# Kernel optimization log

Hardware: AMD Instinct MI355X
Metric: run time of the kernel (lower is better)

Reference implementation:

```python
import jax, jax.numpy as jnp
import numpy as np
from jax import lax

# static dims (match init_kwargs)
B, F, C, H, W = 10, 64, 3, 180, 180   # batch=10 (hard-coded by reshape), arr_size frames
CH, OUT, NCLS = 64, 256, 5            # channel, out_size, len(ansmap)+1
K1, K2, POOL = 9, 5, 2                # second*diff, third, pool
EPS = 1e-5


def setup_inputs() -> dict:
    key = jax.random.key(0)
    ks = jax.random.split(key, 12)
    s = lambda k, shape: jax.random.normal(k, shape, dtype=jnp.float32) * 0.05
    return {
        "x": jax.random.normal(ks[0], (B, F, C, H, W), dtype=jnp.float32),
        "W1": s(ks[1], (CH, C, K1, K1)),
        "b1": s(ks[2], (CH,)),
        "W2": s(ks[3], (3, CH, K2, K2)),
        "b2": s(ks[4], (3,)),
        "gamma": jnp.ones((F,), jnp.float32),
        "beta": jnp.zeros((F,), jnp.float32),
        "Wih": s(ks[5], (3, OUT, 1)),
        "Whh": s(ks[6], (3, OUT, OUT)),
        "bih": s(ks[7], (3, OUT)),
        "bhh": s(ks[8], (3, OUT)),
        "Wl": s(ks[9], (NCLS, OUT)),
        "bl": s(ks[10], (NCLS,)),
    }


def _maxpool2(y):
    return lax.reduce_window(y, -jnp.inf, lax.max, (1, 1, POOL, POOL), (1, 1, POOL, POOL), 'VALID')


def reference(x, W1, b1, W2, b2, gamma, beta, Wih, Whh, bih, bhh, Wl, bl):
    # conv stack applied per frame; batch all B*F frames at once
    xc = x.reshape(B * F, C, H, W)
    y = lax.conv_general_dilated(xc, W1, (K1, K1), 'VALID') + b1[None, :, None, None]
    y = _maxpool2(jax.nn.relu(y))                      # [B*F, CH, 10, 10]
    y = lax.conv_general_dilated(y, W2, (K2, K2), 'VALID') + b2[None, :, None, None]
    y = _maxpool2(jax.nn.relu(y))                      # [B*F, 3, 1, 1]
    y = y.reshape(B, F, 3)

    # BatchNorm1d(arr_size) in train mode: normalize each of the F channels over (batch, length)
    mean = y.mean(axis=(0, 2), keepdims=True)
    var = y.var(axis=(0, 2), keepdims=True)
    y = (y - mean) / jnp.sqrt(var + EPS) * gamma[None, :, None] + beta[None, :, None]

    # per-sample reorder of the 3 channels by (max - min) range over time
    t = y.transpose(0, 2, 1)                           # [B, 3, F]
    rng = t.max(-1) - t.min(-1)                        # [B, 3]
    perm = jnp.argsort(rng, axis=1)                    # [B, 3]
    ts = jnp.take_along_axis(t, perm[:, :, None], axis=1)  # [B, 3, F]

    # rank r goes through RNN r; vmap the scan over the 3 RNNs
    seqs = ts.transpose(1, 2, 0)[..., None]            # [3, F, B, 1]

    def rnn_last(seq, wih, whh, bi, bh):               # seq: [F, B, 1]
        def step(h, xt):
            return jnp.tanh(xt @ wih.T + bi + h @ whh.T + bh), None
        h, _ = lax.scan(step, jnp.zeros((B, OUT), seq.dtype), seq)
        return h                                       # last hidden == output at t=-1

    lasts = jax.vmap(rnn_last)(seqs, Wih, Whh, bih, bhh)  # [3, B, OUT]
    avg = lasts.mean(axis=0)                           # AvgPool2d((3,1)) + Flatten -> [B, OUT]
    return avg @ Wl.T + bl                             # [B, NCLS]
```

## Files before the change

kernel.cpp:

```cpp
#include <hip/hip_runtime.h>

typedef __attribute__((ext_vector_type(8))) short bf16x8;
typedef __attribute__((ext_vector_type(4))) float f32x4;

#define MFMA16(a,b,c) __builtin_amdgcn_mfma_f32_16x16x32_bf16((a),(b),(c),0,0,0)

#define AS1 __attribute__((address_space(1)))
#define AS3 __attribute__((address_space(3)))
__device__ __forceinline__ void async16(void* lds, const void* g){
  __builtin_amdgcn_global_load_lds((const AS1 unsigned int*)g, (AS3 unsigned int*)lds, 16, 0, 0);
}

__device__ __forceinline__ unsigned short f2bf(float f){
  unsigned int u = __float_as_uint(f);
  unsigned int r = (u + 0x7fffu + ((u>>16)&1u)) >> 16;
  return (unsigned short)r;
}
__device__ __forceinline__ float bf2f(unsigned short h){
  return __uint_as_float(((unsigned int)h)<<16);
}
__device__ __forceinline__ float tanh_fast(float x){
  float e = __expf(2.f*x);
  return 1.f - 2.f/(e + 1.f);
}

#define WS_W1H   0u
#define WS_W1L   32768u
#define WS_WHHH  65536u
#define WS_WHHL  458752u
#define WS_Y1    851968u
#define WS_Y2    17235968u
#define WS_LAST  17255936u

__global__ __launch_bounds__(256) void k_prep(const float* __restrict__ W1,
                                              const float* __restrict__ Whh,
                                              unsigned short* __restrict__ w1h,
                                              unsigned short* __restrict__ w1l,
                                              unsigned short* __restrict__ whh_h,
                                              unsigned short* __restrict__ whh_l){
  int t = blockIdx.x*256 + threadIdx.x;
  if (t < 2048){
    int l = t & 63, kt = (t>>6)&7, mt = t>>9;
    int co = mt*16 + (l&15);
    int k0 = kt*32 + ((l>>4)<<3);
    bf16x8 hv, lv;
    #pragma unroll
    for (int j=0;j<8;j++){
      int k = k0 + j;
      float v = (k < 243) ? W1[co*243 + k] : 0.f;
      unsigned short h = f2bf(v);
      unsigned short lo = f2bf(v - bf2f(h));
      hv[j] = (short)h; lv[j] = (short)lo;
    }
    *(bf16x8*)(w1h + (size_t)t*8) = hv;
    *(bf16x8*)(w1l + (size_t)t*8) = lv;
  } else if (t < 2048 + 24576){
    int u = t - 2048;
    int l = u & 63, kt = (u>>6)&7, nt = (u>>9)&15, rnn = u>>13;
    int o = nt*16 + (l&15);
    int k0 = kt*32 + ((l>>4)<<3);
    const float* src = Whh + ((size_t)rnn*256 + o)*256;
    bf16x8 hv, lv;
    #pragma unroll
    for (int j=0;j<8;j++){
      float v = src[k0 + j];
      unsigned short h = f2bf(v);
      unsigned short lo = f2bf(v - bf2f(h));
      hv[j] = (short)h; lv[j] = (short)lo;
    }
    *(bf16x8*)(whh_h + (size_t)u*8) = hv;
    *(bf16x8*)(whh_l + (size_t)u*8) = lv;
  }
}

__global__ __launch_bounds__(256,2) void k_conv1(const float* __restrict__ x,
                                                 const float* __restrict__ b1,
                                                 const unsigned short* __restrict__ w1h,
                                                 const unsigned short* __restrict__ w1l,
                                                 float* __restrict__ y1){
  __shared__ __align__(16) char smem[79840];
  int fr = blockIdx.x / 10, g = blockIdx.x % 10;
  int t = threadIdx.x, w = t>>6, l = t&63;

  const float4* xb4 = (const float4*)x + (size_t)fr*24300 + (size_t)g*810;
  for (int i=t; i<2430; i+=256){
    int c = i/810;
    int rem = i - c*810;
    async16(smem + 40960 + i*16, (const void*)(xb4 + c*8100 + rem));
  }

  bf16x8 ah[8], al[8];
  #pragma unroll
  for (int kt=0; kt<8; kt++){
    size_t fi = (((size_t)(w*8 + kt))*64 + l)*8;
    ah[kt] = *(const bf16x8*)(w1h + fi);
    al[kt] = *(const bf16x8*)(w1l + fi);
  }
  float bias[4];
  #pragma unroll
  for (int reg=0;reg<4;reg++) bias[reg] = b1[w*16 + ((l>>4)<<2) + reg];

  for (int i=t; i<520; i+=256){
    int p = i/13, k = 243 + (i - p*13);
    int off = ((p<<9) + (k<<1)) ^ ((p&7)<<4);
    *(unsigned short*)(smem + off) = 0;
    *(unsigned short*)(smem + 20480 + off) = 0;
  }
  __syncthreads();

  for (int i=t; i<2430; i+=256){
    int c = i/810;
    int rem = i - c*810;
    int rl = rem/45;
    int quad = rem - rl*45;
    int oyl = (rl >= 9) ? 1 : 0;
    int ky = rl - 9*oyl;
    float4 v4 = *(const float4*)(smem + 40960 + i*16);
    int kbase = c*81 + ky*9;
    int col0 = quad<<2;
    int ox = (col0*57)>>9;
    int kx = col0 - 9*ox;
    int p = oyl*20 + ox;
    float vv[4] = {v4.x, v4.y, v4.z, v4.w};
    #pragma unroll
    for (int q=0;q<4;q++){
      int k = kbase + kx;
      int off = ((p<<9) + (k<<1)) ^ ((p&7)<<4);
      unsigned int u = __float_as_uint(vv[q]);
      *(unsigned short*)(smem + off) = (unsigned short)(u>>16);
      float lof = vv[q] - __uint_as_float(u & 0xffff0000u);
      *(unsigned short*)(smem + 20480 + off) = (unsigned short)(__float_as_uint(lof)>>16);
      kx++; if (kx==9){ kx=0; p++; }
    }
  }
  __syncthreads();

  const int pbase[3] = {0, 16, 24};
  int colb = (l>>4)<<4;
  f32x4 acc[3];
  #pragma unroll
  for (int nt=0;nt<3;nt++) acc[nt] = (f32x4){0.f,0.f,0.f,0.f};
  #pragma unroll
  for (int nt=0; nt<3; nt++){
    int p = pbase[nt] + (l&15);
    int sw = (p&7)<<4;
    #pragma unroll
    for (int kt=0; kt<8; kt++){
      int off = ((p<<9) + (kt<<6) + colb) ^ sw;
      bf16x8 bh  = *(const bf16x8*)(smem + off);
      bf16x8 blo = *(const bf16x8*)(smem + 20480 + off);
      acc[nt] = MFMA16(ah[kt], bh,  acc[nt]);
      acc[nt] = MFMA16(ah[kt], blo, acc[nt]);
      acc[nt] = MFMA16(al[kt], bh,  acc[nt]);
    }
  }
  __syncthreads();

  float* poolb = (float*)smem;
  #pragma unroll
  for (int nt=0;nt<3;nt++){
    int m = l&15;
    int p = pbase[nt] + m;
    #pragma unroll
    for (int reg=0;reg<4;reg++){
      int co = w*16 + ((l>>4)<<2) + reg;
      float v = fmaxf(acc[nt][reg] + bias[reg], 0.f);
      if (nt != 2 || m >= 8) poolb[co*41 + p] = v;
    }
  }
  __syncthreads();
  for (int idx=t; idx<640; idx+=256){
    int co = idx/10, xp = idx - co*10;
    const float* pb = poolb + co*41;
    float m = fmaxf(fmaxf(pb[2*xp], pb[2*xp+1]), fmaxf(pb[20+2*xp], pb[21+2*xp]));
    y1[(size_t)fr*6400 + co*100 + g*10 + xp] = m;
  }
}

__global__ __launch_bounds__(256) void k_conv2(const float* __restrict__ y1,
                                               const float* __restrict__ W2,
                                               const float* __restrict__ b2,
                                               float* __restrict__ y2){
  __shared__ __align__(16) float yl[6400];
  __shared__ __align__(16) float w2s[4800];
  int fr = blockIdx.x, t = threadIdx.x;
  const float4* src = (const float4*)(y1 + (size_t)fr*6400);
  for (int i=t;i<1600;i+=256) async16(((float4*)yl) + i, (const void*)(src + i));
  for (int i=t;i<1200;i+=256) async16(((float4*)w2s) + i, (const void*)(((const float4*)W2) + i));
  __syncthreads();
  if (t < 192){
    int o = t>>4, l16 = t&15;
    int ch = o>>2, pos = o&3;
    int oy = pos>>1, ox = pos&1;
    float s = 0.f;
    for (int i=0;i<100;i++){
      int k = l16 + (i<<4);
      int ci = k/25; int r = k - ci*25; int ky = r/5, kx = r - ky*5;
      s += yl[ci*100 + (5*oy+ky)*10 + 5*ox + kx] * w2s[ch*1600 + k];
    }
    #pragma unroll
    for (int d=1; d<16; d<<=1) s += __shfl_xor(s, d);
    float v = fmaxf(s + b2[ch], 0.f);
    v = fmaxf(v, __shfl_xor(v, 16));
    v = fmaxf(v, __shfl_xor(v, 32));
    if ((t&63)==0) y2[fr*3 + (t>>6)] = v;
  }
}

__global__ __launch_bounds__(512) void k_rnn(const unsigned short* __restrict__ whh_h,
                                             const unsigned short* __restrict__ whh_l,
                                             const float* __restrict__ y2,
                                             const float* __restrict__ gamma,
                                             const float* __restrict__ beta,
                                             const float* __restrict__ Wih,
                                             const float* __restrict__ bih,
                                             const float* __restrict__ bhh,
                                             float* __restrict__ lasts){
  __shared__ __align__(16) char hsm[36864];
  float* yl   = (float*)hsm;
  float* af   = (float*)(hsm + 7680);
  float* bfv  = (float*)(hsm + 7936);
  float* rngL = (float*)(hsm + 8192);
  int*   perm = (int*)(hsm + 8320);
  float* tsb  = (float*)(hsm + 8448);
  float* seqL = (float*)(hsm + 32768);
  int rnn = blockIdx.x;
  int t = threadIdx.x, w = t>>6, l = t&63;

  bf16x8 Bh[2][8], Bl[2][8];
  #pragma unroll
  for (int q=0;q<2;q++){
    int nt = 2*w + q;
    #pragma unroll
    for (int kt=0;kt<8;kt++){
      size_t fi = (((((size_t)rnn*16 + nt)*8) + kt)*64 + l)*8;
      Bh[q][kt] = *(const bf16x8*)(whh_h + fi);
      Bl[q][kt] = *(const bf16x8*)(whh_l + fi);
    }
  }
  int o0 = (2*w)*16 + (l&15), o1 = o0 + 16;
  float wih0 = Wih[rnn*256 + o0], wih1 = Wih[rnn*256 + o1];
  float bs0 = bih[rnn*256+o0] + bhh[rnn*256+o0];
  float bs1 = bih[rnn*256+o1] + bhh[rnn*256+o1];

  for (int i=t;i<1920;i+=512) yl[i] = y2[i];
  __syncthreads();
  if (t < 64){
    float mu = 0.f;
    for (int b=0;b<10;b++)
      for (int ch=0;ch<3;ch++) mu += yl[(b*64 + t)*3 + ch];
    mu *= (1.f/30.f);
    float v = 0.f;
    for (int b=0;b<10;b++)
      for (int ch=0;ch<3;ch++){ float d = yl[(b*64+t)*3+ch] - mu; v += d*d; }
    v *= (1.f/30.f);
    float rs = rsqrtf(v + 1e-5f);
    float a = gamma[t]*rs;
    af[t] = a; bfv[t] = beta[t] - mu*a;
  }
  __syncthreads();
  if (t < 30){
    int b = t/3, ch = t - b*3;
    float mx = -1e30f, mn = 1e30f;
    for (int f=0; f<64; f++){
      float v = yl[(b*64+f)*3+ch]*af[f] + bfv[f];
      tsb[(b*3+ch)*64 + f] = v;
      mx = fmaxf(mx, v); mn = fminf(mn, v);
    }
    rngL[b*3+ch] = mx - mn;
  }
  __syncthreads();
  if (t < 10){
    #pragma unroll
    for (int ch=0; ch<3; ch++){
      float rc = rngL[t*3+ch];
      int rank = 0;
      #pragma unroll
      for (int c2=0; c2<3; c2++){
        float r2 = rngL[t*3+c2];
        if (r2 < rc || (r2 == rc && c2 < ch)) rank++;
      }
      perm[t*3+rank] = ch;
    }
  }
  __syncthreads();
  for (int i=t;i<1024;i+=512){
    int step = i>>4, b = i&15;
    float v = 0.f;
    if (b < 10){ int p = perm[b*3 + rnn]; v = tsb[(b*3+p)*64 + step]; }
    seqL[i] = v;
  }
  __syncthreads();

  float4 z4 = {0.f,0.f,0.f,0.f};
  for (int i=t; i<1024; i+=512) ((float4*)hsm)[i] = z4;
  __syncthreads();
  int arow = l&15, colb = (l>>4)<<4, sw = (arow&7)<<4;
  int b_base = (l>>4)<<2;
  for (int step=0; step<64; step++){
    char* cur = hsm + ((step&1)<<14);
    char* nxt = hsm + (((step+1)&1)<<14);
    f32x4 p0=(f32x4){0,0,0,0}, q0=p0, r0=p0, p1=p0, q1=p0, r1=p0;
    #pragma unroll
    for (int kt=0; kt<8; kt++){
      int off = ((arow<<9) + (kt<<6) + colb) ^ sw;
      bf16x8 ahv = *(const bf16x8*)(cur + off);
      bf16x8 alv = *(const bf16x8*)(cur + 8192 + off);
      p0 = MFMA16(ahv, Bh[0][kt], p0);
      q0 = MFMA16(ahv, Bl[0][kt], q0);
      r0 = MFMA16(alv, Bh[0][kt], r0);
      p1 = MFMA16(ahv, Bh[1][kt], p1);
      q1 = MFMA16(ahv, Bl[1][kt], q1);
      r1 = MFMA16(alv, Bh[1][kt], r1);
    }
    float4 sx = *(const float4*)(seqL + (step<<4) + b_base);
    float sxa[4] = {sx.x, sx.y, sx.z, sx.w};
    #pragma unroll
    for (int reg=0; reg<4; reg++){
      int b = b_base + reg;
      float a0 = (p0[reg] + q0[reg]) + r0[reg];
      float a1 = (p1[reg] + q1[reg]) + r1[reg];
      float h0 = tanh_fast(a0 + sxa[reg]*wih0 + bs0);
      float h1 = tanh_fast(a1 + sxa[reg]*wih1 + bs1);
      int wsw = (b&7)<<4;
      int off0 = ((b<<9) + (o0<<1)) ^ wsw;
      int off1 = ((b<<9) + (o1<<1)) ^ wsw;
      unsigned int u0 = __float_as_uint(h0);
      unsigned int u1 = __float_as_uint(h1);
      *(unsigned short*)(nxt + off0) = (unsigned short)(u0>>16);
      float l0 = h0 - __uint_as_float(u0 & 0xffff0000u);
      *(unsigned short*)(nxt + 8192 + off0) = (unsigned short)(__float_as_uint(l0)>>16);
      *(unsigned short*)(nxt + off1) = (unsigned short)(u1>>16);
      float l1 = h1 - __uint_as_float(u1 & 0xffff0000u);
      *(unsigned short*)(nxt + 8192 + off1) = (unsigned short)(__float_as_uint(l1)>>16);
      if (step == 63){
        lasts[((size_t)rnn*16 + b)*256 + o0] = h0;
        lasts[((size_t)rnn*16 + b)*256 + o1] = h1;
      }
    }
    __syncthreads();
  }
}

__global__ __launch_bounds__(512) void k_head(const float* __restrict__ lasts,
                                              const float* __restrict__ Wl,
                                              const float* __restrict__ bl,
                                              float* __restrict__ out){
  int t = threadIdx.x;
  if (t < 400){
    int oidx = t>>3, l8 = t&7;
    int b = oidx/5, c = oidx - b*5;
    float s = 0.f;
    for (int i=0;i<32;i++){
      int o = (l8<<5) + i;
      float avg = (lasts[(size_t)(0*16+b)*256+o] + lasts[(size_t)(1*16+b)*256+o]
                 + lasts[(size_t)(2*16+b)*256+o]) * (1.f/3.f);
      s += avg * Wl[c*256 + o];
    }
    #pragma unroll
    for (int d=1; d<8; d<<=1) s += __shfl_xor(s, d);
    if (l8 == 0) out[oidx] = s + bl[c];
  }
}

extern "C" void kernel_launch(void* const* d_in, const int* in_sizes, int n_in,
                              void* d_out, int out_size, void* d_ws, size_t ws_size,
                              hipStream_t stream){
  const float* x    = (const float*)d_in[0];
  const float* W1   = (const float*)d_in[1];
  const float* b1   = (const float*)d_in[2];
  const float* W2   = (const float*)d_in[3];
  const float* b2   = (const float*)d_in[4];
  const float* gamma= (const float*)d_in[5];
  const float* beta = (const float*)d_in[6];
  const float* Wih  = (const float*)d_in[7];
  const float* Whh  = (const float*)d_in[8];
  const float* bih  = (const float*)d_in[9];
  const float* bhh  = (const float*)d_in[10];
  const float* Wl   = (const float*)d_in[11];
  const float* bl   = (const float*)d_in[12];
  char* ws = (char*)d_ws;
  unsigned short* w1h  = (unsigned short*)(ws + WS_W1H);
  unsigned short* w1l  = (unsigned short*)(ws + WS_W1L);
  unsigned short* whhh = (unsigned short*)(ws + WS_WHHH);
  unsigned short* whhl = (unsigned short*)(ws + WS_WHHL);
  float* y1   = (float*)(ws + WS_Y1);
  float* y2   = (float*)(ws + WS_Y2);
  float* last = (float*)(ws + WS_LAST);

  hipLaunchKernelGGL(k_prep,  dim3(104),  dim3(256), 0, stream, W1, Whh, w1h, w1l, whhh, whhl);
  hipLaunchKernelGGL(k_conv1, dim3(6400), dim3(256), 0, stream, x, b1, w1h, w1l, y1);
  hipLaunchKernelGGL(k_conv2, dim3(640),  dim3(256), 0, stream, y1, W2, b2, y2);
  hipLaunchKernelGGL(k_rnn,   dim3(3),    dim3(512), 0, stream, whhh, whhl, y2, gamma, beta, Wih, bih, bhh, last);
  hipLaunchKernelGGL(k_head,  dim3(1),    dim3(512), 0, stream, last, Wl, bl, (float*)d_out);
}
```

Baseline: 204.2 us.

## Shrink conv1 LDS footprint by processing output rows in two halves with register prefetch

The conv1 kernel now stages only one output row (20 positions) of im2col data at a time, cutting shared memory from about 80KB to 20KB and raising the launch-bounds occupancy hint from 2 to 8 blocks. Input is loaded straight into registers instead of being copied into an LDS staging buffer, and the second row's loads are issued before the first row's MFMAs to overlap latency. Max-pooling now uses lane shuffles and a register max across the two row passes, replacing the LDS pool buffer. The cost is more registers per thread, an extra barrier round, and two MFMA passes that each cover two overlapping position tiles.

```diff
diff --git a/kernel.cpp b/kernel.cpp
--- a/kernel.cpp
+++ b/kernel.cpp
@@ -73,107 +73,157 @@
   }
 }
 
-__global__ __launch_bounds__(256,2) void k_conv1(const float* __restrict__ x,
+__global__ __launch_bounds__(256,8) void k_conv1(const float* __restrict__ x,
                                                  const float* __restrict__ b1,
                                                  const unsigned short* __restrict__ w1h,
                                                  const unsigned short* __restrict__ w1l,
                                                  float* __restrict__ y1){
-  __shared__ __align__(16) char smem[79840];
-  int fr = blockIdx.x / 10, g = blockIdx.x % 10;
+  __shared__ __align__(16) char smem[20480];
+  int fr = blockIdx.x/10, g = blockIdx.x%10;
   int t = threadIdx.x, w = t>>6, l = t&63;
 
-  const float4* xb4 = (const float4*)x + (size_t)fr*24300 + (size_t)g*810;
-  for (int i=t; i<2430; i+=256){
-    int c = i/810;
-    int rem = i - c*810;
-    async16(smem + 40960 + i*16, (const void*)(xb4 + c*8100 + rem));
-  }
-
   bf16x8 ah[8], al[8];
   #pragma unroll
-  for (int kt=0; kt<8; kt++){
-    size_t fi = (((size_t)(w*8 + kt))*64 + l)*8;
-    ah[kt] = *(const bf16x8*)(w1h + fi);
-    al[kt] = *(const bf16x8*)(w1l + fi);
+  for (int kt=0;kt<8;kt++){
+    size_t fi = (((size_t)(w*8+kt))*64 + l)*8;
+    ah[kt] = *(const bf16x8*)(w1h+fi);
+    al[kt] = *(const bf16x8*)(w1l+fi);
   }
   float bias[4];
   #pragma unroll
   for (int reg=0;reg<4;reg++) bias[reg] = b1[w*16 + ((l>>4)<<2) + reg];
 
-  for (int i=t; i<520; i+=256){
-    int p = i/13, k = 243 + (i - p*13);
-    int off = ((p<<9) + (k<<1)) ^ ((p&7)<<4);
-    *(unsigned short*)(smem + off) = 0;
-    *(unsigned short*)(smem + 20480 + off) = 0;
-  }
-  __syncthreads();
-
-  for (int i=t; i<2430; i+=256){
-    int c = i/810;
-    int rem = i - c*810;
-    int rl = rem/45;
-    int quad = rem - rl*45;
-    int oyl = (rl >= 9) ? 1 : 0;
-    int ky = rl - 9*oyl;
-    float4 v4 = *(const float4*)(smem + 40960 + i*16);
-    int kbase = c*81 + ky*9;
+  const float4* xb = (const float4*)x + (size_t)fr*24300;
+  int rowbase = g*18;
+
+  float4 rv[5]; int pp[5], kk[5], kxv[5]; bool okv[5];
+  #pragma unroll
+  for (int ii=0; ii<5; ii++){
+    int i = t + (ii<<8);
+    okv[ii] = (i < 1215);
+    int c = i/405, rem = i - c*405;
+    int ky = rem/45, quad = rem - ky*45;
     int col0 = quad<<2;
     int ox = (col0*57)>>9;
-    int kx = col0 - 9*ox;
-    int p = oyl*20 + ox;
-    float vv[4] = {v4.x, v4.y, v4.z, v4.w};
-    #pragma unroll
-    for (int q=0;q<4;q++){
-      int k = kbase + kx;
-      int off = ((p<<9) + (k<<1)) ^ ((p&7)<<4);
-      unsigned int u = __float_as_uint(vv[q]);
-      *(unsigned short*)(smem + off) = (unsigned short)(u>>16);
-      float lof = vv[q] - __uint_as_float(u & 0xffff0000u);
-      *(unsigned short*)(smem + 20480 + off) = (unsigned short)(__float_as_uint(lof)>>16);
-      kx++; if (kx==9){ kx=0; p++; }
-    }
-  }
-  __syncthreads();
-
-  const int pbase[3] = {0, 16, 24};
-  int colb = (l>>4)<<4;
-  f32x4 acc[3];
-  #pragma unroll
-  for (int nt=0;nt<3;nt++) acc[nt] = (f32x4){0.f,0.f,0.f,0.f};
-  #pragma unroll
-  for (int nt=0; nt<3; nt++){
-    int p = pbase[nt] + (l&15);
-    int sw = (p&7)<<4;
-    #pragma unroll
-    for (int kt=0; kt<8; kt++){
-      int off = ((p<<9) + (kt<<6) + colb) ^ sw;
-      bf16x8 bh  = *(const bf16x8*)(smem + off);
-      bf16x8 blo = *(const bf16x8*)(smem + 20480 + off);
-      acc[nt] = MFMA16(ah[kt], bh,  acc[nt]);
-      acc[nt] = MFMA16(ah[kt], blo, acc[nt]);
-      acc[nt] = MFMA16(al[kt], bh,  acc[nt]);
-    }
-  }
-  __syncthreads();
-
-  float* poolb = (float*)smem;
-  #pragma unroll
-  for (int nt=0;nt<3;nt++){
-    int m = l&15;
-    int p = pbase[nt] + m;
-    #pragma unroll
-    for (int reg=0;reg<4;reg++){
-      int co = w*16 + ((l>>4)<<2) + reg;
-      float v = fmaxf(acc[nt][reg] + bias[reg], 0.f);
-      if (nt != 2 || m >= 8) poolb[co*41 + p] = v;
-    }
-  }
-  __syncthreads();
-  for (int idx=t; idx<640; idx+=256){
-    int co = idx/10, xp = idx - co*10;
-    const float* pb = poolb + co*41;
-    float m = fmaxf(fmaxf(pb[2*xp], pb[2*xp+1]), fmaxf(pb[20+2*xp], pb[21+2*xp]));
-    y1[(size_t)fr*6400 + co*100 + g*10 + xp] = m;
+    kxv[ii] = col0 - 9*ox;
+    pp[ii] = ox;
+    kk[ii] = c*81 + ky*9;
+    int gi = c*8100 + (rowbase + ky)*45 + quad;
+    rv[ii] = okv[ii] ? xb[gi] : (float4){0.f,0.f,0.f,0.f};
+  }
+  for (int i=t; i<260; i+=256){
+    int p = i/13, k = 243 + (i - p*13);
+    int off = ((p<<9)+(k<<1)) ^ ((p&7)<<4);
+    *(unsigned short*)(smem+off) = 0;
+    *(unsigned short*)(smem+10240+off) = 0;
+  }
+  #pragma unroll
+  for (int ii=0; ii<5; ii++){
+    if (okv[ii]){
+      int p = pp[ii], kx = kxv[ii];
+      float vv[4] = {rv[ii].x, rv[ii].y, rv[ii].z, rv[ii].w};
+      #pragma unroll
+      for (int q=0;q<4;q++){
+        int k = kk[ii] + kx;
+        int off = ((p<<9)+(k<<1)) ^ ((p&7)<<4);
+        unsigned int u = __float_as_uint(vv[q]);
+        *(unsigned short*)(smem+off) = (unsigned short)(u>>16);
+        float lof = vv[q] - __uint_as_float(u & 0xffff0000u);
+        *(unsigned short*)(smem+10240+off) = (unsigned short)(__float_as_uint(lof)>>16);
+        kx++; if (kx==9){ kx=0; p++; }
+      }
+    }
+  }
+  __syncthreads();
+
+  #pragma unroll
+  for (int ii=0; ii<5; ii++){
+    int i = t + (ii<<8);
+    int c = i/405, rem = i - c*405;
+    int ky = rem/45, quad = rem - ky*45;
+    int gi = c*8100 + (rowbase + 9 + ky)*45 + quad;
+    rv[ii] = okv[ii] ? xb[gi] : (float4){0.f,0.f,0.f,0.f};
+  }
+
+  int m = l&15, colb = (l>>4)<<4;
+  int p0 = m, p1 = 4+m;
+  int sw0 = (p0&7)<<4, sw1 = (p1&7)<<4;
+  f32x4 acc0 = (f32x4){0.f,0.f,0.f,0.f}, acc1 = acc0;
+  #pragma unroll
+  for (int kt=0;kt<8;kt++){
+    int off0 = ((p0<<9)+(kt<<6)+colb) ^ sw0;
+    int off1 = ((p1<<9)+(kt<<6)+colb) ^ sw1;
+    bf16x8 bh0 = *(const bf16x8*)(smem+off0);
+    bf16x8 bl0 = *(const bf16x8*)(smem+10240+off0);
+    bf16x8 bh1 = *(const bf16x8*)(smem+off1);
+    bf16x8 bl1 = *(const bf16x8*)(smem+10240+off1);
+    acc0 = MFMA16(ah[kt], bh0, acc0);
+    acc0 = MFMA16(ah[kt], bl0, acc0);
+    acc0 = MFMA16(al[kt], bh0, acc0);
+    acc1 = MFMA16(ah[kt], bh1, acc1);
+    acc1 = MFMA16(ah[kt], bl1, acc1);
+    acc1 = MFMA16(al[kt], bh1, acc1);
+  }
+  float vA0[4], vA1[4];
+  #pragma unroll
+  for (int reg=0;reg<4;reg++){
+    float v0 = fmaxf(acc0[reg]+bias[reg], 0.f);
+    vA0[reg] = fmaxf(v0, __shfl_xor(v0,1));
+    float v1 = fmaxf(acc1[reg]+bias[reg], 0.f);
+    vA1[reg] = fmaxf(v1, __shfl_xor(v1,1));
+  }
+  __syncthreads();
+
+  #pragma unroll
+  for (int ii=0; ii<5; ii++){
+    if (okv[ii]){
+      int p = pp[ii], kx = kxv[ii];
+      float vv[4] = {rv[ii].x, rv[ii].y, rv[ii].z, rv[ii].w};
+      #pragma unroll
+      for (int q=0;q<4;q++){
+        int k = kk[ii] + kx;
+        int off = ((p<<9)+(k<<1)) ^ ((p&7)<<4);
+        unsigned int u = __float_as_uint(vv[q]);
+        *(unsigned short*)(smem+off) = (unsigned short)(u>>16);
+        float lof = vv[q] - __uint_as_float(u & 0xffff0000u);
+        *(unsigned short*)(smem+10240+off) = (unsigned short)(__float_as_uint(lof)>>16);
+        kx++; if (kx==9){ kx=0; p++; }
+      }
+    }
+  }
+  __syncthreads();
+
+  acc0 = (f32x4){0.f,0.f,0.f,0.f}; acc1 = acc0;
+  #pragma unroll
+  for (int kt=0;kt<8;kt++){
+    int off0 = ((p0<<9)+(kt<<6)+colb) ^ sw0;
+    int off1 = ((p1<<9)+(kt<<6)+colb) ^ sw1;
+    bf16x8 bh0 = *(const bf16x8*)(smem+off0);
+    bf16x8 bl0 = *(const bf16x8*)(smem+10240+off0);
+    bf16x8 bh1 = *(const bf16x8*)(smem+off1);
+    bf16x8 bl1 = *(const bf16x8*)(smem+10240+off1);
+    acc0 = MFMA16(ah[kt], bh0, acc0);
+    acc0 = MFMA16(ah[kt], bl0, acc0);
+    acc0 = MFMA16(al[kt], bh0, acc0);
+    acc1 = MFMA16(ah[kt], bh1, acc1);
+    acc1 = MFMA16(ah[kt], bl1, acc1);
+    acc1 = MFMA16(al[kt], bh1, acc1);
+  }
+  size_t ybase = (size_t)fr*6400 + g*10;
+  #pragma unroll
+  for (int reg=0;reg<4;reg++){
+    int co = w*16 + ((l>>4)<<2) + reg;
+    float v0 = fmaxf(acc0[reg]+bias[reg], 0.f);
+    v0 = fmaxf(v0, __shfl_xor(v0,1));
+    float r0 = fmaxf(vA0[reg], v0);
+    float v1 = fmaxf(acc1[reg]+bias[reg], 0.f);
+    v1 = fmaxf(v1, __shfl_xor(v1,1));
+    float r1 = fmaxf(vA1[reg], v1);
+    if ((m&1)==0){
+      y1[ybase + co*100 + (m>>1)] = r0;
+      if (m >= 12)
+        y1[ybase + co*100 + ((4+m)>>1)] = r1;
+    }
   }
 }
 
```

New measurement: 453.7 us. +122.1%, slower.
